# Kernel tuning notes

Hardware: AMD Instinct MI355X
Metric: run time of the kernel (lower is better)

## Reference

```python
import jax, jax.numpy as jnp
import numpy as np

DIM = 512
H = 8
D = 64
EPS = 1e-5


def _ln(x, g, b):
    m = jnp.mean(x, axis=-1, keepdims=True)
    v = jnp.var(x, axis=-1, keepdims=True)
    return (x - m) * jax.lax.rsqrt(v + EPS) * g + b


def _attn(x, ctx, wq, wk, wv, wo, bo):
    B, S, _ = x.shape
    T = ctx.shape[1]
    q = (x @ wq).reshape(B, S, H, D)
    k = (ctx @ wk).reshape(B, T, H, D)
    v = (ctx @ wv).reshape(B, T, H, D)
    scale = D ** -0.5
    score = jnp.einsum('bqhd,bkhd->bhqk', q, k) * scale  # [B,H,S,T]
    w = jax.nn.softmax(score, axis=-1)
    o = jnp.einsum('bhqk,bkhd->bqhd', w, v).reshape(B, S, H * D)
    return o @ wo + bo


def _geglu(x, w, b):
    h = x @ w + b
    y, gate = h[..., :4 * DIM], h[..., 4 * DIM:]
    tanh_res = jnp.tanh(gate * 0.7978845608 * (1.0 + 0.044715 * gate * gate))
    return y * 0.5 * gate * (1.0 + tanh_res)


def setup_inputs() -> dict:
    key = jax.random.key(0)
    ks = jax.random.split(key, 16)
    s = 0.02
    inp = {
        'x': jax.random.normal(ks[0], (2, 4096, DIM), jnp.float32),
        'context': jax.random.normal(ks[1], (2, 77, DIM), jnp.float32),
        'ln1_g': jnp.ones((DIM,), jnp.float32),
        'ln1_b': jnp.zeros((DIM,), jnp.float32),
        'wq1': jax.random.normal(ks[2], (DIM, H * D), jnp.float32) * s,
        'wk1': jax.random.normal(ks[3], (DIM, H * D), jnp.float32) * s,
        'wv1': jax.random.normal(ks[4], (DIM, H * D), jnp.float32) * s,
        'wo1': jax.random.normal(ks[5], (H * D, H * D), jnp.float32) * s,
        'bo1': jnp.zeros((H * D,), jnp.float32),
        'ln2_g': jnp.ones((DIM,), jnp.float32),
        'ln2_b': jnp.zeros((DIM,), jnp.float32),
        'wq2': jax.random.normal(ks[6], (DIM, H * D), jnp.float32) * s,
        'wk2': jax.random.normal(ks[7], (DIM, H * D), jnp.float32) * s,
        'wv2': jax.random.normal(ks[8], (DIM, H * D), jnp.float32) * s,
        'wo2': jax.random.normal(ks[9], (H * D, H * D), jnp.float32) * s,
        'bo2': jnp.zeros((H * D,), jnp.float32),
        'ln3_g': jnp.ones((DIM,), jnp.float32),
        'ln3_b': jnp.zeros((DIM,), jnp.float32),
        'geglu_w': jax.random.normal(ks[10], (DIM, 8 * DIM), jnp.float32) * s,
        'geglu_b': jnp.zeros((8 * DIM,), jnp.float32),
        'out_w': jax.random.normal(ks[11], (4 * DIM, DIM), jnp.float32) * s,
        'out_b': jnp.zeros((DIM,), jnp.float32),
    }
    return inp


def reference(x, context, ln1_g, ln1_b, wq1, wk1, wv1, wo1, bo1,
              ln2_g, ln2_b, wq2, wk2, wv2, wo2, bo2,
              ln3_g, ln3_b, geglu_w, geglu_b, out_w, out_b):
    h = _attn(_ln(x, ln1_g, ln1_b), _ln(x, ln1_g, ln1_b), wq1, wk1, wv1, wo1, bo1) + x
    h = _attn(_ln(h, ln2_g, ln2_b), context, wq2, wk2, wv2, wo2, bo2) + h
    ff = _geglu(_ln(h, ln3_g, ln3_b), geglu_w, geglu_b)
    return ff @ out_w + out_b + h
```

## Files before the change

### kernel.cpp

```cpp
#include <hip/hip_runtime.h>
#include <hip/hip_bf16.h>
#include <math.h>

#define DIM 512
#define NHEAD 8
#define HD 64
#define BATCH 2
#define SEQ 4096
#define CTXLEN 77
#define NTOK (BATCH*SEQ)
#define NCTX (BATCH*CTXLEN)

typedef __hip_bfloat16 bf16;
typedef __attribute__((ext_vector_type(8))) short bf8_t;
typedef __attribute__((ext_vector_type(4))) float f4_t;

__device__ __forceinline__ float b2f(bf16 v){ return __bfloat162float(v); }
__device__ __forceinline__ bf16  f2b(float v){ return __float2bfloat16(v); }
__device__ __forceinline__ unsigned int packbf2(float a, float b){
    unsigned int au = __float_as_uint(a) + 0x8000u;
    unsigned int bu = __float_as_uint(b) + 0x8000u;
    return __builtin_amdgcn_perm(bu, au, 0x07060302u);
}
__device__ __forceinline__ void  stf(float* p, float v){ *p = v; }
__device__ __forceinline__ void  stf(bf16* p, float v){ *p = f2b(v); }

__global__ __launch_bounds__(256)
void ln_kernel(const float* __restrict__ x, const float* __restrict__ g,
               const float* __restrict__ b, bf16* __restrict__ out, int nrows)
{
    int row  = blockIdx.x * 4 + (threadIdx.x >> 6);
    int lane = threadIdx.x & 63;
    if (row >= nrows) return;
    const float* xr = x + (size_t)row * DIM;
    float v[8];
    float s = 0.f, sq = 0.f;
    #pragma unroll
    for (int j = 0; j < 8; ++j) {
        float f = xr[lane + 64*j];
        v[j] = f; s += f; sq += f*f;
    }
    #pragma unroll
    for (int off = 32; off; off >>= 1) {
        s  += __shfl_xor(s,  off);
        sq += __shfl_xor(sq, off);
    }
    float mean = s * (1.f/DIM);
    float var  = sq * (1.f/DIM) - mean*mean;
    float rstd = rsqrtf(var + 1e-5f);
    bf16* orow = out + (size_t)row * DIM;
    #pragma unroll
    for (int j = 0; j < 8; ++j) {
        int c = lane + 64*j;
        orow[c] = f2b((v[j]-mean)*rstd*g[c] + b[c]);
    }
}

struct PrepArgs {
    const float* src8[8]; bf16* dst8[8];
    const float* gw; bf16* gwT;
    const float* ow; bf16* owT;
    const float* ctx; bf16* ctxb;
};
__global__ __launch_bounds__(256)
void prep_kernel(PrepArgs a)
{
    __shared__ float tile[32][33];
    const int bid = blockIdx.x;
    const int tx = threadIdx.x & 31, ty = threadIdx.x >> 5;
    const float* W; bf16* Wt; int K, N, n0, k0;
    if (bid < 2048) {
        int z = bid >> 8, t = bid & 255;
        W = a.src8[z]; Wt = a.dst8[z]; K = 512; N = 512;
        n0 = (t & 15)*32; k0 = (t >> 4)*32;
    } else if (bid < 4096) {
        int t = bid - 2048;
        W = a.gw; Wt = a.gwT; K = 512; N = 4096;
        n0 = (t & 127)*32; k0 = (t >> 7)*32;
    } else if (bid < 5120) {
        int t = bid - 4096;
        W = a.ow; Wt = a.owT; K = 2048; N = 512;
        n0 = (t & 15)*32; k0 = (t >> 4)*32;
    } else {
        int i = (bid - 5120)*256 + threadIdx.x;
        a.ctxb[i] = f2b(a.ctx[i]);
        return;
    }
    #pragma unroll
    for (int p = 0; p < 4; ++p)
        tile[ty + p*8][tx] = W[(size_t)(k0 + ty + p*8)*N + n0 + tx];
    __syncthreads();
    #pragma unroll
    for (int p = 0; p < 4; ++p)
        Wt[(size_t)(n0 + ty + p*8)*K + k0 + tx] = f2b(tile[tx][ty + p*8]);
}

__global__ __launch_bounds__(256)
void v_transpose_kernel(const bf16* __restrict__ V, bf16* __restrict__ Vt, int T, int pitch)
{
    __shared__ __align__(16) unsigned short tile[64*64];
    const int tid = threadIdx.x;
    const int b = blockIdx.z, h = blockIdx.y;
    const int t0 = blockIdx.x * 64;
    #pragma unroll
    for (int it = 0; it < 2; ++it) {
        int e = tid + it*256;
        int t = e >> 3, c = e & 7;
        int gk = t0 + t;
        bf8_t v = {0,0,0,0,0,0,0,0};
        if (gk < T) v = *(const bf8_t*)(V + ((size_t)(b*T + gk))*DIM + h*HD + c*8);
        *(bf8_t*)&tile[t*64 + c*8] = v;
    }
    __syncthreads();
    #pragma unroll
    for (int it = 0; it < 2; ++it) {
        int e = tid + it*256;
        int d = e & 63, oc = e >> 6;
        unsigned short tmp[8];
        #pragma unroll
        for (int j = 0; j < 8; ++j) tmp[j] = tile[(oc*8 + j)*64 + d];
        *(bf8_t*)(Vt + ((size_t)((b*8 + h)*64 + d))*pitch + t0 + oc*8) = *(bf8_t*)tmp;
    }
}

struct OutPtrs { void* p[3]; };
template<int RESID, typename OUTT, bool GUARD, bool VT>
__global__ __launch_bounds__(256)
void gemm_mfma_kernel(const bf16* __restrict__ A, const bf16* __restrict__ Wt,
                      const float* __restrict__ bias, const float* __restrict__ resid,
                      OutPtrs outs, int M, int K)
{
    __shared__ __align__(16) unsigned short As[128*64];
    __shared__ __align__(16) unsigned short Bs[64*64];
    const int tid  = threadIdx.x;
    const int wave = tid >> 6, lane = tid & 63;
    const int l16  = lane & 15, quad = lane >> 4;
    const int wm = (wave >> 1) * 64, wn = (wave & 1) * 32;
    const int m0 = blockIdx.y * 128, n0 = blockIdx.x * 64;
    OUTT* outp = (OUTT*)outs.p[n0 >> 9];
    const int lc0 = n0 & 511;
    const int sr = tid >> 3, sc_ = tid & 7;

    f4_t acc[4][2];
    #pragma unroll
    for (int i = 0; i < 4; ++i) { acc[i][0] = f4_t{0,0,0,0}; acc[i][1] = f4_t{0,0,0,0}; }

    bf8_t pa[4], pb[2];
    #pragma unroll
    for (int p = 0; p < 4; ++p) {
        int r = sr + p*32;
        int gr = m0 + r;
        if (GUARD) gr = (gr < M) ? gr : (M-1);
        pa[p] = *(const bf8_t*)(A + (size_t)gr*K + sc_*8);
    }
    #pragma unroll
    for (int p = 0; p < 2; ++p)
        pb[p] = *(const bf8_t*)(Wt + (size_t)(n0 + sr + p*32)*K + sc_*8);

    for (int k0 = 0; k0 < K; k0 += 64) {
        #pragma unroll
        for (int p = 0; p < 4; ++p) {
            int r = sr + p*32;
            *(bf8_t*)&As[r*64 + ((sc_ ^ (r&7))*8)] = pa[p];
        }
        #pragma unroll
        for (int p = 0; p < 2; ++p) {
            int r = sr + p*32;
            *(bf8_t*)&Bs[r*64 + ((sc_ ^ (r&7))*8)] = pb[p];
        }
        __syncthreads();
        if (k0 + 64 < K) {
            #pragma unroll
            for (int p = 0; p < 4; ++p) {
                int r = sr + p*32;
                int gr = m0 + r;
                if (GUARD) gr = (gr < M) ? gr : (M-1);
                pa[p] = *(const bf8_t*)(A + (size_t)gr*K + k0 + 64 + sc_*8);
            }
            #pragma unroll
            for (int p = 0; p < 2; ++p)
                pb[p] = *(const bf8_t*)(Wt + (size_t)(n0 + sr + p*32)*K + k0 + 64 + sc_*8);
        }
        #pragma unroll
        for (int kc = 0; kc < 2; ++kc) {
            const int cg = kc*4 + quad;
            bf8_t af[4], bfr[2];
            #pragma unroll
            for (int mt = 0; mt < 4; ++mt) {
                int r = wm + mt*16 + l16;
                af[mt] = *(const bf8_t*)&As[r*64 + ((cg ^ (r&7))*8)];
            }
            #pragma unroll
            for (int nt = 0; nt < 2; ++nt) {
                int r = wn + nt*16 + l16;
                bfr[nt] = *(const bf8_t*)&Bs[r*64 + ((cg ^ (r&7))*8)];
            }
            #pragma unroll
            for (int mt = 0; mt < 4; ++mt)
                #pragma unroll
                for (int nt = 0; nt < 2; ++nt)
                    acc[mt][nt] = __builtin_amdgcn_mfma_f32_16x16x32_bf16(af[mt], bfr[nt], acc[mt][nt], 0, 0, 0);
        }
        __syncthreads();
    }

    if (VT && (n0 >> 9) == 2) {
        bf16* vt = (bf16*)outs.p[2];
        #pragma unroll
        for (int mt = 0; mt < 4; ++mt) {
            int row = m0 + wm + mt*16 + quad*4;
            int bb = row >> 12, tok = row & 4095;
            #pragma unroll
            for (int nt = 0; nt < 2; ++nt) {
                int c = lc0 + wn + nt*16 + l16;
                int h = c >> 6, d = c & 63;
                uint2 w;
                w.x = packbf2(acc[mt][nt][0], acc[mt][nt][1]);
                w.y = packbf2(acc[mt][nt][2], acc[mt][nt][3]);
                *(uint2*)(vt + ((size_t)((bb*8 + h)*64 + d))*SEQ + tok) = w;
            }
        }
        return;
    }

    #pragma unroll
    for (int mt = 0; mt < 4; ++mt) {
        #pragma unroll
        for (int r_ = 0; r_ < 4; ++r_) {
            int row = m0 + wm + mt*16 + quad*4 + r_;
            if (GUARD && row >= M) continue;
            size_t rb = (size_t)row * 512;
            #pragma unroll
            for (int nt = 0; nt < 2; ++nt) {
                int col = lc0 + wn + nt*16 + l16;
                float v = acc[mt][nt][r_];
                if (bias) v += bias[col];
                if (RESID) v += resid[rb + col];
                stf(&outp[rb + col], v);
            }
        }
    }
}

__global__ __launch_bounds__(256)
void geglu_mfma_kernel(const bf16* __restrict__ A, const bf16* __restrict__ WtG,
                       const float* __restrict__ bias, bf16* __restrict__ outp)
{
    __shared__ __align__(16) unsigned short As[128*64];
    __shared__ __align__(16) unsigned short Bys[64*64];
    __shared__ __align__(16) unsigned short Bgs[64*64];
    const int tid  = threadIdx.x;
    const int wave = tid >> 6, lane = tid & 63;
    const int l16  = lane & 15, quad = lane >> 4;
    const int m0 = blockIdx.y * 128, n0 = blockIdx.x * 64;
    const int sr = tid >> 3, sc_ = tid & 7;

    f4_t accy[2][4], accg[2][4];
    #pragma unroll
    for (int i = 0; i < 2; ++i)
        #pragma unroll
        for (int j = 0; j < 4; ++j) { accy[i][j] = f4_t{0,0,0,0}; accg[i][j] = f4_t{0,0,0,0}; }

    bf8_t pa[4], py[2], pg[2];
    #pragma unroll
    for (int p = 0; p < 4; ++p)
        pa[p] = *(const bf8_t*)(A + (size_t)(m0 + sr + p*32)*DIM + sc_*8);
    #pragma unroll
    for (int p = 0; p < 2; ++p) {
        py[p] = *(const bf8_t*)(WtG + (size_t)(n0 + sr + p*32)*DIM + sc_*8);
        pg[p] = *(const bf8_t*)(WtG + (size_t)(2048 + n0 + sr + p*32)*DIM + sc_*8);
    }

    for (int k0 = 0; k0 < DIM; k0 += 64) {
        #pragma unroll
        for (int p = 0; p < 4; ++p) {
            int r = sr + p*32;
            *(bf8_t*)&As[r*64 + ((sc_ ^ (r&7))*8)] = pa[p];
        }
        #pragma unroll
        for (int p = 0; p < 2; ++p) {
            int r = sr + p*32;
            *(bf8_t*)&Bys[r*64 + ((sc_ ^ (r&7))*8)] = py[p];
            *(bf8_t*)&Bgs[r*64 + ((sc_ ^ (r&7))*8)] = pg[p];
        }
        __syncthreads();
        if (k0 + 64 < DIM) {
            #pragma unroll
            for (int p = 0; p < 4; ++p)
                pa[p] = *(const bf8_t*)(A + (size_t)(m0 + sr + p*32)*DIM + k0 + 64 + sc_*8);
            #pragma unroll
            for (int p = 0; p < 2; ++p) {
                py[p] = *(const bf8_t*)(WtG + (size_t)(n0 + sr + p*32)*DIM + k0 + 64 + sc_*8);
                pg[p] = *(const bf8_t*)(WtG + (size_t)(2048 + n0 + sr + p*32)*DIM + k0 + 64 + sc_*8);
            }
        }
        #pragma unroll
        for (int kc = 0; kc < 2; ++kc) {
            const int cg = kc*4 + quad;
            bf8_t af[2];
            #pragma unroll
            for (int mt = 0; mt < 2; ++mt) {
                int r = wave*32 + mt*16 + l16;
                af[mt] = *(const bf8_t*)&As[r*64 + ((cg ^ (r&7))*8)];
            }
            #pragma unroll
            for (int nt = 0; nt < 4; ++nt) {
                int r = nt*16 + l16;
                bf8_t by = *(const bf8_t*)&Bys[r*64 + ((cg ^ (r&7))*8)];
                bf8_t bg = *(const bf8_t*)&Bgs[r*64 + ((cg ^ (r&7))*8)];
                #pragma unroll
                for (int mt = 0; mt < 2; ++mt) {
                    accy[mt][nt] = __builtin_amdgcn_mfma_f32_16x16x32_bf16(af[mt], by, accy[mt][nt], 0, 0, 0);
                    accg[mt][nt] = __builtin_amdgcn_mfma_f32_16x16x32_bf16(af[mt], bg, accg[mt][nt], 0, 0, 0);
                }
            }
        }
        __syncthreads();
    }

    #pragma unroll
    for (int mt = 0; mt < 2; ++mt) {
        #pragma unroll
        for (int r_ = 0; r_ < 4; ++r_) {
            int row = m0 + wave*32 + mt*16 + quad*4 + r_;
            size_t rb = (size_t)row * 2048;
            #pragma unroll
            for (int nt = 0; nt < 4; ++nt) {
                int col = n0 + nt*16 + l16;
                float y = accy[mt][nt][r_] + bias[col];
                float g = accg[mt][nt][r_] + bias[2048 + col];
                float t = tanhf(0.7978845608f*g*(1.f + 0.044715f*g*g));
                outp[rb + col] = f2b(y * 0.5f * g * (1.f + t));
            }
        }
    }
}

__global__ __launch_bounds__(512)
void attn_mfma_kernel(const bf16* __restrict__ Qm, const bf16* __restrict__ Km,
                      const bf16* __restrict__ VtG, bf16* __restrict__ Om,
                      int T, int vpitch)
{
    __shared__ __align__(16) unsigned short Ks[64*64];
    __shared__ __align__(16) unsigned short Vts[64*64];
    __shared__ __align__(16) unsigned short Ps[8][16*64];

    const int tid  = threadIdx.x;
    const int wave = tid >> 6, lane = tid & 63;
    const int l16  = lane & 15, quad = lane >> 4;
    const int b = blockIdx.z, h = blockIdx.y;
    const int qblk = blockIdx.x * 128;
    const int sr = tid >> 3, sc_ = tid & 7;

    bf8_t ones;
    #pragma unroll
    for (int j = 0; j < 8; ++j) ((unsigned short*)&ones)[j] = 0x3F80;

    bf8_t qf[2];
    {
        const bf16* qp = Qm + ((size_t)(b*SEQ + qblk + wave*16 + l16))*DIM + h*HD + quad*8;
        #pragma unroll
        for (int kc = 0; kc < 2; ++kc) {
            bf8_t v = *(const bf8_t*)(qp + kc*32);
            unsigned short* u = (unsigned short*)&v;
            unsigned int* w = (unsigned int*)&v;
            #pragma unroll
            for (int j = 0; j < 4; ++j) {
                float f0 = b2f(*(bf16*)&u[2*j])   * 0.1803368801f;
                float f1 = b2f(*(bf16*)&u[2*j+1]) * 0.1803368801f;
                w[j] = packbf2(f0, f1);
            }
            qf[kc] = v;
        }
    }

    f4_t o[4];
    #pragma unroll
    for (int dt = 0; dt < 4; ++dt) o[dt] = f4_t{0,0,0,0};
    f4_t lacc = {0,0,0,0};

    const bf16* Kbase = Km + (size_t)b*T*DIM + h*HD;
    const bf16* Vbase = VtG + ((size_t)((b*8 + h)*64 + sr))*vpitch;

    bf8_t kq, vq;
    kq = bf8_t{0,0,0,0,0,0,0,0};
    if (sr < T) kq = *(const bf8_t*)(Kbase + (size_t)sr*DIM + sc_*8);
    vq = *(const bf8_t*)(Vbase + sc_*8);

    const int ntiles = (T + 63) >> 6;
    for (int t0 = 0; t0 < ntiles; ++t0) {
        const int kb = t0 << 6;
        *(bf8_t*)&Ks[sr*64 + ((sc_ ^ (sr&7))*8)]  = kq;
        *(bf8_t*)&Vts[sr*64 + ((sc_ ^ (sr&7))*8)] = vq;
        __syncthreads();
        if (t0 + 1 < ntiles) {
            int gk = kb + 64 + sr;
            kq = bf8_t{0,0,0,0,0,0,0,0};
            if (gk < T) kq = *(const bf8_t*)(Kbase + (size_t)gk*DIM + sc_*8);
            vq = *(const bf8_t*)(Vbase + kb + 64 + sc_*8);
        }

        bf8_t kf[4][2], vf[4][2];
        #pragma unroll
        for (int t = 0; t < 4; ++t) {
            int r = t*16 + l16;
            #pragma unroll
            for (int kc = 0; kc < 2; ++kc) {
                int cg = kc*4 + quad;
                kf[t][kc] = *(const bf8_t*)&Ks[r*64 + ((cg ^ (r&7))*8)];
                vf[t][kc] = *(const bf8_t*)&Vts[r*64 + ((cg ^ (r&7))*8)];
            }
        }
        const bool tail = (kb + 64 > T);

        f4_t sc4[4];
        #pragma unroll
        for (int km = 0; km < 4; ++km) {
            f4_t c = {0,0,0,0};
            c = __builtin_amdgcn_mfma_f32_16x16x32_bf16(kf[km][0], qf[0], c, 0, 0, 0);
            c = __builtin_amdgcn_mfma_f32_16x16x32_bf16(kf[km][1], qf[1], c, 0, 0, 0);
            sc4[km] = c;
        }
        if (tail) {
            #pragma unroll
            for (int km = 0; km < 4; ++km)
                #pragma unroll
                for (int r = 0; r < 4; ++r)
                    if (kb + km*16 + quad*4 + r >= T) sc4[km][r] = -1e30f;
        }
        #pragma unroll
        for (int km = 0; km < 4; ++km) {
            uint2 w;
            w.x = packbf2(exp2f(sc4[km][0]), exp2f(sc4[km][1]));
            w.y = packbf2(exp2f(sc4[km][2]), exp2f(sc4[km][3]));
            int chunk = 2*km + (quad >> 1);
            int a = l16*64 + ((chunk ^ (l16 & 7))*8) + (quad & 1)*4;
            *(uint2*)&Ps[wave][a] = w;
        }
        #pragma unroll
        for (int kc = 0; kc < 2; ++kc) {
            int cg = kc*4 + quad;
            bf8_t pf = *(const bf8_t*)&Ps[wave][l16*64 + ((cg ^ (l16 & 7))*8)];
            lacc = __builtin_amdgcn_mfma_f32_16x16x32_bf16(ones, pf, lacc, 0, 0, 0);
            #pragma unroll
            for (int dt = 0; dt < 4; ++dt)
                o[dt] = __builtin_amdgcn_mfma_f32_16x16x32_bf16(vf[dt][kc], pf, o[dt], 0, 0, 0);
        }
        __syncthreads();
    }

    {
        float inv = 1.f / lacc[0];
        int tok = qblk + wave*16 + l16;
        size_t base = ((size_t)(b*SEQ + tok))*DIM + h*HD;
        #pragma unroll
        for (int dt = 0; dt < 4; ++dt) {
            uint2 w;
            w.x = packbf2(o[dt][0]*inv, o[dt][1]*inv);
            w.y = packbf2(o[dt][2]*inv, o[dt][3]*inv);
            *(uint2*)(Om + base + dt*16 + quad*4) = w;
        }
    }
}

extern "C" void kernel_launch(void* const* d_in, const int* in_sizes, int n_in,
                              void* d_out, int out_size, void* d_ws, size_t ws_size,
                              hipStream_t stream)
{
    (void)in_sizes; (void)n_in; (void)out_size; (void)ws_size;
    const float* x    = (const float*)d_in[0];
    const float* ctx  = (const float*)d_in[1];
    const float* ln1g = (const float*)d_in[2];
    const float* ln1b = (const float*)d_in[3];
    const float* wq1  = (const float*)d_in[4];
    const float* wk1  = (const float*)d_in[5];
    const float* wv1  = (const float*)d_in[6];
    const float* wo1  = (const float*)d_in[7];
    const float* bo1  = (const float*)d_in[8];
    const float* ln2g = (const float*)d_in[9];
    const float* ln2b = (const float*)d_in[10];
    const float* wq2  = (const float*)d_in[11];
    const float* wk2  = (const float*)d_in[12];
    const float* wv2  = (const float*)d_in[13];
    const float* wo2  = (const float*)d_in[14];
    const float* bo2  = (const float*)d_in[15];
    const float* ln3g = (const float*)d_in[16];
    const float* ln3b = (const float*)d_in[17];
    const float* gw   = (const float*)d_in[18];
    const float* gb   = (const float*)d_in[19];
    const float* ow   = (const float*)d_in[20];
    const float* ob   = (const float*)d_in[21];
    float* out = (float*)d_out;

    char* ws = (char*)d_ws;
    bf16* An  = (bf16*)(ws);
    bf16* Qb  = (bf16*)(ws + ((size_t)8<<20));
    bf16* Kb  = (bf16*)(ws + ((size_t)16<<20));
    bf16* Vb  = (bf16*)(ws + ((size_t)24<<20));
    bf16* Ob  = (bf16*)(ws + ((size_t)32<<20));
    bf16* FF  = Qb;
    float* Hf = out;
    bf16* WT  = (bf16*)(ws + ((size_t)40<<20));
    bf16* wq1T = WT + 0*262144, *wk1T = WT + 1*262144, *wv1T = WT + 2*262144, *wo1T = WT + 3*262144;
    bf16* wq2T = WT + 4*262144, *wk2T = WT + 5*262144, *wv2T = WT + 6*262144, *wo2T = WT + 7*262144;
    bf16* gwT  = (bf16*)(ws + ((size_t)44<<20));
    bf16* owT  = (bf16*)(ws + ((size_t)48<<20));
    bf16* ctxb = (bf16*)(ws + ((size_t)50<<20));
    bf16* VtG2 = (bf16*)(ws + ((size_t)50<<20) + ((size_t)512<<10));
    bf16* VtG  = (bf16*)(ws + ((size_t)52<<20));

    dim3 blk(256);
    dim3 blkA(512);

    PrepArgs pa;
    pa.src8[0]=wq1; pa.src8[1]=wk1; pa.src8[2]=wv1; pa.src8[3]=wo1;
    pa.src8[4]=wq2; pa.src8[5]=wk2; pa.src8[6]=wv2; pa.src8[7]=wo2;
    pa.dst8[0]=wq1T; pa.dst8[1]=wk1T; pa.dst8[2]=wv1T; pa.dst8[3]=wo1T;
    pa.dst8[4]=wq2T; pa.dst8[5]=wk2T; pa.dst8[6]=wv2T; pa.dst8[7]=wo2T;
    pa.gw=gw; pa.gwT=gwT; pa.ow=ow; pa.owT=owT; pa.ctx=ctx; pa.ctxb=ctxb;
    prep_kernel<<<dim3(5428), blk, 0, stream>>>(pa);

    dim3 gLN(NTOK/4);
    dim3 gQKV(24, 64);
    dim3 gG(8, 64);
    dim3 gKVx(16, 2);
    dim3 gGEGLU(32, 64);
    dim3 gATT(SEQ/128, NHEAD, BATCH);
    OutPtrs oQKV{{Qb, Kb, VtG}};
    OutPtrs oKVx{{Kb, Vb, nullptr}};
    OutPtrs oQ{{Qb, nullptr, nullptr}};
    OutPtrs oH{{Hf, nullptr, nullptr}};
    OutPtrs oOut{{out, nullptr, nullptr}};

    ln_kernel<<<gLN, blk, 0, stream>>>(x, ln1g, ln1b, An, NTOK);
    gemm_mfma_kernel<0,bf16,false,true><<<gQKV, blk, 0, stream>>>(An, wq1T, nullptr, nullptr, oQKV, NTOK, DIM);
    attn_mfma_kernel<<<gATT, blkA, 0, stream>>>(Qb, Kb, VtG, Ob, SEQ, SEQ);
    gemm_mfma_kernel<1,float,false,false><<<gG, blk, 0, stream>>>(Ob, wo1T, bo1, x, oH, NTOK, DIM);

    ln_kernel<<<gLN, blk, 0, stream>>>(Hf, ln2g, ln2b, An, NTOK);
    gemm_mfma_kernel<0,bf16,false,false><<<gG, blk, 0, stream>>>(An, wq2T, nullptr, nullptr, oQ, NTOK, DIM);
    gemm_mfma_kernel<0,bf16,true,false><<<gKVx, blk, 0, stream>>>(ctxb, wk2T, nullptr, nullptr, oKVx, NCTX, DIM);
    v_transpose_kernel<<<dim3(2, NHEAD, BATCH), blk, 0, stream>>>(Vb, VtG2, CTXLEN, 128);
    attn_mfma_kernel<<<gATT, blkA, 0, stream>>>(Qb, Kb, VtG2, Ob, CTXLEN, 128);
    gemm_mfma_kernel<1,float,false,false><<<gG, blk, 0, stream>>>(Ob, wo2T, bo2, Hf, oH, NTOK, DIM);

    ln_kernel<<<gLN, blk, 0, stream>>>(Hf, ln3g, ln3b, An, NTOK);
    geglu_mfma_kernel<<<gGEGLU, blk, 0, stream>>>(An, gwT, gb, FF);
    gemm_mfma_kernel<1,float,false,false><<<gG, blk, 0, stream>>>(FF, owT, ob, Hf, oOut, NTOK, 2048);
}
```

Baseline: 452.3 us.

## Widen attention KV tile to 128, fuse LN1 into prep and V-transpose into GEMM

The attention kernel now processes 128 keys per shared-memory tile, split into two 64-key halves, which halves the number of barriers and loop iterations. The cost is doubled LDS use, which can reduce occupancy. The first LayerNorm moves into the prep kernel and the context V projection writes its transposed layout directly from the GEMM epilogue, removing two kernel launches. The new transposed store is scalar and uncoalesced, but it is small.

```diff
diff --git a/kernel.cpp b/kernel.cpp
--- a/kernel.cpp
+++ b/kernel.cpp
@@ -25,42 +25,12 @@
 __device__ __forceinline__ void  stf(float* p, float v){ *p = v; }
 __device__ __forceinline__ void  stf(bf16* p, float v){ *p = f2b(v); }
 
-__global__ __launch_bounds__(256)
-void ln_kernel(const float* __restrict__ x, const float* __restrict__ g,
-               const float* __restrict__ b, bf16* __restrict__ out, int nrows)
-{
-    int row  = blockIdx.x * 4 + (threadIdx.x >> 6);
-    int lane = threadIdx.x & 63;
-    if (row >= nrows) return;
-    const float* xr = x + (size_t)row * DIM;
-    float v[8];
-    float s = 0.f, sq = 0.f;
-    #pragma unroll
-    for (int j = 0; j < 8; ++j) {
-        float f = xr[lane + 64*j];
-        v[j] = f; s += f; sq += f*f;
-    }
-    #pragma unroll
-    for (int off = 32; off; off >>= 1) {
-        s  += __shfl_xor(s,  off);
-        sq += __shfl_xor(sq, off);
-    }
-    float mean = s * (1.f/DIM);
-    float var  = sq * (1.f/DIM) - mean*mean;
-    float rstd = rsqrtf(var + 1e-5f);
-    bf16* orow = out + (size_t)row * DIM;
-    #pragma unroll
-    for (int j = 0; j < 8; ++j) {
-        int c = lane + 64*j;
-        orow[c] = f2b((v[j]-mean)*rstd*g[c] + b[c]);
-    }
-}
-
 struct PrepArgs {
     const float* src8[8]; bf16* dst8[8];
     const float* gw; bf16* gwT;
     const float* ow; bf16* owT;
     const float* ctx; bf16* ctxb;
+    const float* x; const float* lng; const float* lnb; bf16* An;
 };
 __global__ __launch_bounds__(256)
 void prep_kernel(PrepArgs a)
@@ -81,10 +51,36 @@
         int t = bid - 4096;
         W = a.ow; Wt = a.owT; K = 2048; N = 512;
         n0 = (t & 15)*32; k0 = (t >> 4)*32;
-    } else {
+    } else if (bid < 5428) {
         int i = (bid - 5120)*256 + threadIdx.x;
         a.ctxb[i] = f2b(a.ctx[i]);
         return;
+    } else {
+        int row  = (bid - 5428)*4 + (threadIdx.x >> 6);
+        int lane = threadIdx.x & 63;
+        const float* xr = a.x + (size_t)row * DIM;
+        float v[8];
+        float s = 0.f, sq = 0.f;
+        #pragma unroll
+        for (int j = 0; j < 8; ++j) {
+            float f = xr[lane + 64*j];
+            v[j] = f; s += f; sq += f*f;
+        }
+        #pragma unroll
+        for (int off = 32; off; off >>= 1) {
+            s  += __shfl_xor(s,  off);
+            sq += __shfl_xor(sq, off);
+        }
+        float mean = s * (1.f/DIM);
+        float var  = sq * (1.f/DIM) - mean*mean;
+        float rstd = rsqrtf(var + 1e-5f);
+        bf16* orow = a.An + (size_t)row * DIM;
+        #pragma unroll
+        for (int j = 0; j < 8; ++j) {
+            int c = lane + 64*j;
+            orow[c] = f2b((v[j]-mean)*rstd*a.lng[c] + a.lnb[c]);
+        }
+        return;
     }
     #pragma unroll
     for (int p = 0; p < 4; ++p)
@@ -96,35 +92,38 @@
 }
 
 __global__ __launch_bounds__(256)
-void v_transpose_kernel(const bf16* __restrict__ V, bf16* __restrict__ Vt, int T, int pitch)
+void ln_kernel(const float* __restrict__ x, const float* __restrict__ g,
+               const float* __restrict__ b, bf16* __restrict__ out, int nrows)
 {
-    __shared__ __align__(16) unsigned short tile[64*64];
-    const int tid = threadIdx.x;
-    const int b = blockIdx.z, h = blockIdx.y;
-    const int t0 = blockIdx.x * 64;
-    #pragma unroll
-    for (int it = 0; it < 2; ++it) {
-        int e = tid + it*256;
-        int t = e >> 3, c = e & 7;
-        int gk = t0 + t;
-        bf8_t v = {0,0,0,0,0,0,0,0};
-        if (gk < T) v = *(const bf8_t*)(V + ((size_t)(b*T + gk))*DIM + h*HD + c*8);
-        *(bf8_t*)&tile[t*64 + c*8] = v;
-    }
-    __syncthreads();
-    #pragma unroll
-    for (int it = 0; it < 2; ++it) {
-        int e = tid + it*256;
-        int d = e & 63, oc = e >> 6;
-        unsigned short tmp[8];
-        #pragma unroll
-        for (int j = 0; j < 8; ++j) tmp[j] = tile[(oc*8 + j)*64 + d];
-        *(bf8_t*)(Vt + ((size_t)((b*8 + h)*64 + d))*pitch + t0 + oc*8) = *(bf8_t*)tmp;
+    int row  = blockIdx.x * 4 + (threadIdx.x >> 6);
+    int lane = threadIdx.x & 63;
+    if (row >= nrows) return;
+    const float* xr = x + (size_t)row * DIM;
+    float v[8];
+    float s = 0.f, sq = 0.f;
+    #pragma unroll
+    for (int j = 0; j < 8; ++j) {
+        float f = xr[lane + 64*j];
+        v[j] = f; s += f; sq += f*f;
+    }
+    #pragma unroll
+    for (int off = 32; off; off >>= 1) {
+        s  += __shfl_xor(s,  off);
+        sq += __shfl_xor(sq, off);
+    }
+    float mean = s * (1.f/DIM);
+    float var  = sq * (1.f/DIM) - mean*mean;
+    float rstd = rsqrtf(var + 1e-5f);
+    bf16* orow = out + (size_t)row * DIM;
+    #pragma unroll
+    for (int j = 0; j < 8; ++j) {
+        int c = lane + 64*j;
+        orow[c] = f2b((v[j]-mean)*rstd*g[c] + b[c]);
     }
 }
 
 struct OutPtrs { void* p[3]; };
-template<int RESID, typename OUTT, bool GUARD, bool VT>
+template<int RESID, typename OUTT, bool GUARD, int VT>
 __global__ __launch_bounds__(256)
 void gemm_mfma_kernel(const bf16* __restrict__ A, const bf16* __restrict__ Wt,
                       const float* __restrict__ bias, const float* __restrict__ resid,
@@ -204,7 +203,7 @@
         __syncthreads();
     }
 
-    if (VT && (n0 >> 9) == 2) {
+    if (VT == 1 && (n0 >> 9) == 2) {
         bf16* vt = (bf16*)outs.p[2];
         #pragma unroll
         for (int mt = 0; mt < 4; ++mt) {
@@ -218,6 +217,26 @@
                 w.x = packbf2(acc[mt][nt][0], acc[mt][nt][1]);
                 w.y = packbf2(acc[mt][nt][2], acc[mt][nt][3]);
                 *(uint2*)(vt + ((size_t)((bb*8 + h)*64 + d))*SEQ + tok) = w;
+            }
+        }
+        return;
+    }
+    if (VT == 2 && (n0 >> 9) == 1) {
+        bf16* vt = (bf16*)outs.p[1];
+        #pragma unroll
+        for (int mt = 0; mt < 4; ++mt) {
+            #pragma unroll
+            for (int r_ = 0; r_ < 4; ++r_) {
+                int row = m0 + wm + mt*16 + quad*4 + r_;
+                if (row >= NCTX) continue;
+                int bb = (row >= CTXLEN) ? 1 : 0;
+                int t  = row - bb*CTXLEN;
+                #pragma unroll
+                for (int nt = 0; nt < 2; ++nt) {
+                    int c = lc0 + wn + nt*16 + l16;
+                    int h = c >> 6, d = c & 63;
+                    vt[((size_t)((bb*8 + h)*64 + d))*128 + t] = f2b(acc[mt][nt][r_]);
+                }
             }
         }
         return;
@@ -341,16 +360,17 @@
                       const bf16* __restrict__ VtG, bf16* __restrict__ Om,
                       int T, int vpitch)
 {
-    __shared__ __align__(16) unsigned short Ks[64*64];
-    __shared__ __align__(16) unsigned short Vts[64*64];
-    __shared__ __align__(16) unsigned short Ps[8][16*64];
+    __shared__ __align__(16) unsigned short Ks[128*64];
+    __shared__ __align__(16) unsigned short Vts[64*128];
+    __shared__ __align__(16) unsigned short Ps[8][16*128];
 
     const int tid  = threadIdx.x;
     const int wave = tid >> 6, lane = tid & 63;
     const int l16  = lane & 15, quad = lane >> 4;
     const int b = blockIdx.z, h = blockIdx.y;
     const int qblk = blockIdx.x * 128;
-    const int sr = tid >> 3, sc_ = tid & 7;
+    const int krow = tid >> 3, kch = tid & 7;
+    const int vrow = tid >> 4, vch = tid & 15;
 
     bf8_t ones;
     #pragma unroll
@@ -380,71 +400,91 @@
     f4_t lacc = {0,0,0,0};
 
     const bf16* Kbase = Km + (size_t)b*T*DIM + h*HD;
-    const bf16* Vbase = VtG + ((size_t)((b*8 + h)*64 + sr))*vpitch;
-
-    bf8_t kq, vq;
-    kq = bf8_t{0,0,0,0,0,0,0,0};
-    if (sr < T) kq = *(const bf8_t*)(Kbase + (size_t)sr*DIM + sc_*8);
-    vq = *(const bf8_t*)(Vbase + sc_*8);
-
-    const int ntiles = (T + 63) >> 6;
+    const bf16* Vbase = VtG + ((size_t)((b*8 + h)*64))*vpitch;
+
+    auto loadKV = [&](int kb, bf8_t* kq, bf8_t* vq) {
+        #pragma unroll
+        for (int it = 0; it < 2; ++it) {
+            int gk = kb + krow + it*64; gk = (gk < T) ? gk : (T-1);
+            kq[it] = *(const bf8_t*)(Kbase + (size_t)gk*DIM + kch*8);
+            int d = vrow + it*32;
+            bf8_t v = *(const bf8_t*)(Vbase + (size_t)d*vpitch + kb + vch*8);
+            if (kb + vch*8 + 8 > T) {
+                #pragma unroll
+                for (int j = 0; j < 8; ++j)
+                    if (kb + vch*8 + j >= T) ((unsigned short*)&v)[j] = 0;
+            }
+            vq[it] = v;
+        }
+    };
+
+    bf8_t kq[2], vq[2];
+    loadKV(0, kq, vq);
+
+    const int ntiles = (T + 127) >> 7;
     for (int t0 = 0; t0 < ntiles; ++t0) {
-        const int kb = t0 << 6;
-        *(bf8_t*)&Ks[sr*64 + ((sc_ ^ (sr&7))*8)]  = kq;
-        *(bf8_t*)&Vts[sr*64 + ((sc_ ^ (sr&7))*8)] = vq;
+        const int kb = t0 << 7;
+        #pragma unroll
+        for (int it = 0; it < 2; ++it) {
+            int r = krow + it*64;
+            *(bf8_t*)&Ks[r*64 + ((kch ^ (r&7))*8)] = kq[it];
+            int rv = vrow + it*32;
+            *(bf8_t*)&Vts[rv*128 + ((vch ^ (rv&7))*8)] = vq[it];
+        }
         __syncthreads();
-        if (t0 + 1 < ntiles) {
-            int gk = kb + 64 + sr;
-            kq = bf8_t{0,0,0,0,0,0,0,0};
-            if (gk < T) kq = *(const bf8_t*)(Kbase + (size_t)gk*DIM + sc_*8);
-            vq = *(const bf8_t*)(Vbase + kb + 64 + sc_*8);
-        }
-
-        bf8_t kf[4][2], vf[4][2];
-        #pragma unroll
-        for (int t = 0; t < 4; ++t) {
-            int r = t*16 + l16;
+        if (t0 + 1 < ntiles) loadKV(kb + 128, kq, vq);
+
+        const bool tail = (kb + 128 > T);
+        #pragma unroll
+        for (int hf = 0; hf < 2; ++hf) {
+            bf8_t kf[4][2];
+            #pragma unroll
+            for (int t = 0; t < 4; ++t) {
+                int r = hf*64 + t*16 + l16;
+                #pragma unroll
+                for (int kc = 0; kc < 2; ++kc) {
+                    int cg = kc*4 + quad;
+                    kf[t][kc] = *(const bf8_t*)&Ks[r*64 + ((cg ^ (r&7))*8)];
+                }
+            }
+            f4_t sc4[4];
+            #pragma unroll
+            for (int km = 0; km < 4; ++km) {
+                f4_t c = {0,0,0,0};
+                c = __builtin_amdgcn_mfma_f32_16x16x32_bf16(kf[km][0], qf[0], c, 0, 0, 0);
+                c = __builtin_amdgcn_mfma_f32_16x16x32_bf16(kf[km][1], qf[1], c, 0, 0, 0);
+                sc4[km] = c;
+            }
+            if (tail) {
+                #pragma unroll
+                for (int km = 0; km < 4; ++km)
+                    #pragma unroll
+                    for (int r = 0; r < 4; ++r)
+                        if (kb + hf*64 + km*16 + quad*4 + r >= T) sc4[km][r] = -1e30f;
+            }
+            #pragma unroll
+            for (int km = 0; km < 4; ++km) {
+                uint2 w;
+                w.x = packbf2(exp2f(sc4[km][0]), exp2f(sc4[km][1]));
+                w.y = packbf2(exp2f(sc4[km][2]), exp2f(sc4[km][3]));
+                int chunk = hf*8 + 2*km + (quad >> 1);
+                int a = l16*128 + ((chunk ^ (l16 & 7))*8) + (quad & 1)*4;
+                *(uint2*)&Ps[wave][a] = w;
+            }
             #pragma unroll
             for (int kc = 0; kc < 2; ++kc) {
                 int cg = kc*4 + quad;
-                kf[t][kc] = *(const bf8_t*)&Ks[r*64 + ((cg ^ (r&7))*8)];
-                vf[t][kc] = *(const bf8_t*)&Vts[r*64 + ((cg ^ (r&7))*8)];
-            }
-        }
-        const bool tail = (kb + 64 > T);
-
-        f4_t sc4[4];
-        #pragma unroll
-        for (int km = 0; km < 4; ++km) {
-            f4_t c = {0,0,0,0};
-            c = __builtin_amdgcn_mfma_f32_16x16x32_bf16(kf[km][0], qf[0], c, 0, 0, 0);
-            c = __builtin_amdgcn_mfma_f32_16x16x32_bf16(kf[km][1], qf[1], c, 0, 0, 0);
-            sc4[km] = c;
-        }
-        if (tail) {
-            #pragma unroll
-            for (int km = 0; km < 4; ++km)
-                #pragma unroll
-                for (int r = 0; r < 4; ++r)
-                    if (kb + km*16 + quad*4 + r >= T) sc4[km][r] = -1e30f;
-        }
-        #pragma unroll
-        for (int km = 0; km < 4; ++km) {
-            uint2 w;
-            w.x = packbf2(exp2f(sc4[km][0]), exp2f(sc4[km][1]));
-            w.y = packbf2(exp2f(sc4[km][2]), exp2f(sc4[km][3]));
-            int chunk = 2*km + (quad >> 1);
-            int a = l16*64 + ((chunk ^ (l16 & 7))*8) + (quad & 1)*4;
-            *(uint2*)&Ps[wave][a] = w;
-        }
-        #pragma unroll
-        for (int kc = 0; kc < 2; ++kc) {
-            int cg = kc*4 + quad;
-            bf8_t pf = *(const bf8_t*)&Ps[wave][l16*64 + ((cg ^ (l16 & 7))*8)];
-            lacc = __builtin_amdgcn_mfma_f32_16x16x32_bf16(ones, pf, lacc, 0, 0, 0);
-            #pragma unroll
-            for (int dt = 0; dt < 4; ++dt)
-                o[dt] = __builtin_amdgcn_mfma_f32_16x16x32_bf16(vf[dt][kc], pf, o[dt], 0, 0, 0);
+                int pc = hf*8 + (cg ^ (l16 & 7));
+                bf8_t pf = *(const bf8_t*)&Ps[wave][l16*128 + pc*8];
+                lacc = __builtin_amdgcn_mfma_f32_16x16x32_bf16(ones, pf, lacc, 0, 0, 0);
+                #pragma unroll
+                for (int dt = 0; dt < 4; ++dt) {
+                    int r = dt*16 + l16;
+                    int vc = hf*8 + (cg ^ (r & 7));
+                    bf8_t vf = *(const bf8_t*)&Vts[r*128 + vc*8];
+                    o[dt] = __builtin_amdgcn_mfma_f32_16x16x32_bf16(vf, pf, o[dt], 0, 0, 0);
+                }
+            }
         }
         __syncthreads();
     }
@@ -496,7 +536,6 @@
     bf16* An  = (bf16*)(ws);
     bf16* Qb  = (bf16*)(ws + ((size_t)8<<20));
     bf16* Kb  = (bf16*)(ws + ((size_t)16<<20));
-    bf16* Vb  = (bf16*)(ws + ((size_t)24<<20));
     bf16* Ob  = (bf16*)(ws + ((size_t)32<<20));
     bf16* FF  = Qb;
     float* Hf = out;
@@ -518,7 +557,8 @@
     pa.dst8[0]=wq1T; pa.dst8[1]=wk1T; pa.dst8[2]=wv1T; pa.dst8[3]=wo1T;
     pa.dst8[4]=wq2T; pa.dst8[5]=wk2T; pa.dst8[6]=wv2T; pa.dst8[7]=wo2T;
     pa.gw=gw; pa.gwT=gwT; pa.ow=ow; pa.owT=owT; pa.ctx=ctx; pa.ctxb=ctxb;
-    prep_kernel<<<dim3(5428), blk, 0, stream>>>(pa);
+    pa.x=x; pa.lng=ln1g; pa.lnb=ln1b; pa.An=An;
+    prep_kernel<<<dim3(7476), blk, 0, stream>>>(pa);
 
     dim3 gLN(NTOK/4);
     dim3 gQKV(24, 64);
@@ -527,24 +567,22 @@
     dim3 gGEGLU(32, 64);
     dim3 gATT(SEQ/128, NHEAD, BATCH);
     OutPtrs oQKV{{Qb, Kb, VtG}};
-    OutPtrs oKVx{{Kb, Vb, nullptr}};
+    OutPtrs oKVx{{Kb, VtG2, nullptr}};
     OutPtrs oQ{{Qb, nullptr, nullptr}};
     OutPtrs oH{{Hf, nullptr, nullptr}};
     OutPtrs oOut{{out, nullptr, nullptr}};
 
-    ln_kernel<<<gLN, blk, 0, stream>>>(x, ln1g, ln1b, An, NTOK);
-    gemm_mfma_kernel<0,bf16,false,true><<<gQKV, blk, 0, stream>>>(An, wq1T, nullptr, nullptr, oQKV, NTOK, DIM);
+    gemm_mfma_kernel<0,bf16,false,1><<<gQKV, blk, 0, stream>>>(An, wq1T, nullptr, nullptr, oQKV, NTOK, DIM);
     attn_mfma_kernel<<<gATT, blkA, 0, stream>>>(Qb, Kb, VtG, Ob, SEQ, SEQ);
-    gemm_mfma_kernel<1,float,false,false><<<gG, blk, 0, stream>>>(Ob, wo1T, bo1, x, oH, NTOK, DIM);
+    gemm_mfma_kernel<1,float,false,0><<<gG, blk, 0, stream>>>(Ob, wo1T, bo1, x, oH, NTOK, DIM);
 
     ln_kernel<<<gLN, blk, 0, stream>>>(Hf, ln2g, ln2b, An, NTOK);
-    gemm_mfma_kernel<0,bf16,false,false><<<gG, blk, 0, stream>>>(An, wq2T, nullptr, nullptr, oQ, NTOK, DIM);
-    gemm_mfma_kernel<0,bf16,true,false><<<gKVx, blk, 0, stream>>>(ctxb, wk2T, nullptr, nullptr, oKVx, NCTX, DIM);
-    v_transpose_kernel<<<dim3(2, NHEAD, BATCH), blk, 0, stream>>>(Vb, VtG2, CTXLEN, 128);
+    gemm_mfma_kernel<0,bf16,false,0><<<gG, blk, 0, stream>>>(An, wq2T, nullptr, nullptr, oQ, NTOK, DIM);
+    gemm_mfma_kernel<0,bf16,true,2><<<gKVx, blk, 0, stream>>>(ctxb, wk2T, nullptr, nullptr, oKVx, NCTX, DIM);
     attn_mfma_kernel<<<gATT, blkA, 0, stream>>>(Qb, Kb, VtG2, Ob, CTXLEN, 128);
-    gemm_mfma_kernel<1,float,false,false><<<gG, blk, 0, stream>>>(Ob, wo2T, bo2, Hf, oH, NTOK, DIM);
+    gemm_mfma_kernel<1,float,false,0><<<gG, blk, 0, stream>>>(Ob, wo2T, bo2, Hf, oH, NTOK, DIM);
 
     ln_kernel<<<gLN, blk, 0, stream>>>(Hf, ln3g, ln3b, An, NTOK);
     geglu_mfma_kernel<<<gGEGLU, blk, 0, stream>>>(An, gwT, gb, FF);
-    gemm_mfma_kernel<1,float,false,false><<<gG, blk, 0, stream>>>(FF, owT, ob, Hf, oOut, NTOK, 2048);
-}
+    gemm_mfma_kernel<1,float,false,0><<<gG, blk, 0, stream>>>(FF, owT, ob, Hf, oOut, NTOK, 2048);
+}
```

After: 455.8 us. No clear change (+0.8%).
